# Kernel tuning notes

Hardware: AMD Instinct MI355X
Metric: run time of the kernel (lower is better)

## Reference

```python
import jax, jax.numpy as jnp
import numpy as np

VOCAB = 100000
EMB = 300
B, L = 2048, 256

def setup_inputs() -> dict:
    key = jax.random.key(0)
    k1, k2, k3, k4 = jax.random.split(key, 4)
    tokens = jax.random.randint(k1, (B, L), 0, VOCAB)
    # lengths in [1, L] (original items always have at least one token)
    lengths = jax.random.randint(k2, (B,), 1, L + 1)
    W_emb = jax.random.normal(k3, (VOCAB, EMB), dtype=jnp.float32)
    fc_w = jax.random.normal(k4, (1, EMB), dtype=jnp.float32) / np.sqrt(EMB)
    fc_b = jnp.zeros((1,), dtype=jnp.float32)
    return {"tokens": tokens, "lengths": lengths, "W_emb": W_emb, "fc_w": fc_w, "fc_b": fc_b}

def reference(tokens, lengths, W_emb, fc_w, fc_b):
    # ragged gather + per-item mean pool, fused via padding mask
    emb = W_emb[tokens]                                   # [B, L, D]
    mask = (jnp.arange(L)[None, :] < lengths[:, None])    # [B, L]
    summed = jnp.einsum('bld,bl->bd', emb, mask.astype(emb.dtype))
    avg = summed / lengths[:, None].astype(emb.dtype)     # [B, D]
    z = avg @ fc_w.T + fc_b                               # [B, 1]
    return jax.nn.sigmoid(z)
```

## Files before the change

kernel.cpp:

```cpp
#include <hip/hip_runtime.h>
#include <hip/hip_bf16.h>

#define VOCAB 100000
#define EMB 300
#define BATCH 2048
#define SEQ 256

__global__ void __launch_bounds__(256) vocab_dot_kernel(
    const float* __restrict__ W, const float* __restrict__ fcw,
    float* __restrict__ p, int nrows) {
  const int lane = threadIdx.x & 63;
  const int wave = (blockIdx.x * blockDim.x + threadIdx.x) >> 6;
  const int nwaves = (gridDim.x * blockDim.x) >> 6;

  const float4* fcw4 = (const float4*)fcw;
  float4 wa = fcw4[lane];
  float4 wb = make_float4(0.f, 0.f, 0.f, 0.f);
  if (lane < 11) wb = fcw4[64 + lane];

  for (int v = wave; v < nrows; v += nwaves) {
    const float4* row = (const float4*)(W + (size_t)v * EMB);
    float4 a = row[lane];
    float acc = a.x * wa.x + a.y * wa.y + a.z * wa.z + a.w * wa.w;
    if (lane < 11) {
      float4 b4 = row[64 + lane];
      acc += b4.x * wb.x + b4.y * wb.y + b4.z * wb.z + b4.w * wb.w;
    }
    #pragma unroll
    for (int off = 32; off > 0; off >>= 1)
      acc += __shfl_down(acc, off, 64);
    if (lane == 0) p[v] = acc;
  }
}

__global__ void __launch_bounds__(256) pool_sigmoid_kernel(
    const int* __restrict__ tokens, const int* __restrict__ lengths,
    const float* __restrict__ p, const float* __restrict__ fcb,
    float* __restrict__ out, int B, int L) {
  const int lane = threadIdx.x & 63;
  const int wib = threadIdx.x >> 6;
  const int b = blockIdx.x * (blockDim.x >> 6) + wib;
  if (b >= B) return;

  const int len = lengths[b];
  const int* t = tokens + (size_t)b * L;
  float acc = 0.f;
  for (int l = lane; l < len; l += 64)
    acc += p[t[l]];
  #pragma unroll
  for (int off = 32; off > 0; off >>= 1)
    acc += __shfl_down(acc, off, 64);
  if (lane == 0) {
    float z = acc / (float)len + fcb[0];
    out[b] = 1.0f / (1.0f + expf(-z));
  }
}

extern "C" void kernel_launch(void* const* d_in, const int* in_sizes, int n_in,
                              void* d_out, int out_size, void* d_ws, size_t ws_size,
                              hipStream_t stream) {
  const int*   tokens  = (const int*)d_in[0];
  const int*   lengths = (const int*)d_in[1];
  const float* W_emb   = (const float*)d_in[2];
  const float* fc_w    = (const float*)d_in[3];
  const float* fc_b    = (const float*)d_in[4];
  float* out = (float*)d_out;
  float* p   = (float*)d_ws;

  vocab_dot_kernel<<<2048, 256, 0, stream>>>(W_emb, fc_w, p, VOCAB);

  pool_sigmoid_kernel<<<BATCH / 4, 256, 0, stream>>>(
      tokens, lengths, p, fc_b, out, BATCH, SEQ);
}
```

Baseline: 30.68 us.

## Fuse gather and dot into one per-item pooling kernel, dropping vocab precompute

```diff
diff --git a/kernel.cpp b/kernel.cpp
--- a/kernel.cpp
+++ b/kernel.cpp
@@ -2,56 +2,65 @@
 #include <hip/hip_bf16.h>
 
 #define VOCAB 100000
-#define EMB 300
+#define EMB   300
 #define BATCH 2048
-#define SEQ 256
+#define SEQ   256
 
-__global__ void __launch_bounds__(256) vocab_dot_kernel(
+typedef float f4 __attribute__((ext_vector_type(4)));
+
+__global__ void __launch_bounds__(256) item_pool_kernel(
+    const int* __restrict__ tokens, const int* __restrict__ lengths,
     const float* __restrict__ W, const float* __restrict__ fcw,
-    float* __restrict__ p, int nrows) {
-  const int lane = threadIdx.x & 63;
-  const int wave = (blockIdx.x * blockDim.x + threadIdx.x) >> 6;
-  const int nwaves = (gridDim.x * blockDim.x) >> 6;
+    const float* __restrict__ fcb, float* __restrict__ out) {
+  __shared__ int   stok[SEQ];
+  __shared__ float spart[16];
+  const int b   = blockIdx.x;
+  const int tid = threadIdx.x;
+  const int i   = tid & 15;
+  const int grp = tid >> 4;
+  const int len = lengths[b];
 
-  const float4* fcw4 = (const float4*)fcw;
-  float4 wa = fcw4[lane];
-  float4 wb = make_float4(0.f, 0.f, 0.f, 0.f);
-  if (lane < 11) wb = fcw4[64 + lane];
+  stok[tid] = tokens[(size_t)b * SEQ + tid];
+  __syncthreads();
 
-  for (int v = wave; v < nrows; v += nwaves) {
-    const float4* row = (const float4*)(W + (size_t)v * EMB);
-    float4 a = row[lane];
-    float acc = a.x * wa.x + a.y * wa.y + a.z * wa.z + a.w * wa.w;
-    if (lane < 11) {
-      float4 b4 = row[64 + lane];
-      acc += b4.x * wb.x + b4.y * wb.y + b4.z * wb.z + b4.w * wb.w;
+  const f4* fcw4 = (const f4*)fcw;
+  const f4 zero = {0.f, 0.f, 0.f, 0.f};
+  const f4 w0 = fcw4[i];
+  const f4 w1 = fcw4[i + 16];
+  const f4 w2 = fcw4[i + 32];
+  const f4 w3 = fcw4[i + 48];
+  const f4 w4 = (i < 11) ? fcw4[i + 64] : zero;
+
+  const int nmine = (len > grp) ? ((len - grp + 15) >> 4) : 0;
+
+  f4 acc = zero;
+  if (nmine > 0) {
+    const f4* r = (const f4*)(W + (size_t)stok[grp] * EMB);
+    f4 A0 = r[i], A1 = r[i + 16], A2 = r[i + 32], A3 = r[i + 48];
+    f4 A4 = (i < 11) ? r[i + 64] : zero;
+    #pragma unroll 2
+    for (int j = 1; j < nmine; ++j) {
+      const f4* r2 = (const f4*)(W + (size_t)stok[grp + (j << 4)] * EMB);
+      f4 B0 = r2[i], B1 = r2[i + 16], B2 = r2[i + 32], B3 = r2[i + 48];
+      f4 B4 = (i < 11) ? r2[i + 64] : zero;
+      acc += A0 * w0 + A1 * w1 + A2 * w2 + A3 * w3 + A4 * w4;
+      A0 = B0; A1 = B1; A2 = B2; A3 = B3; A4 = B4;
     }
+    acc += A0 * w0 + A1 * w1 + A2 * w2 + A3 * w3 + A4 * w4;
+  }
+
+  float s = acc.x + acc.y + acc.z + acc.w;
+  s += __shfl_xor(s, 8, 16);
+  s += __shfl_xor(s, 4, 16);
+  s += __shfl_xor(s, 2, 16);
+  s += __shfl_xor(s, 1, 16);
+  if (i == 0) spart[grp] = s;
+  __syncthreads();
+  if (tid == 0) {
+    float t = 0.f;
     #pragma unroll
-    for (int off = 32; off > 0; off >>= 1)
-      acc += __shfl_down(acc, off, 64);
-    if (lane == 0) p[v] = acc;
-  }
-}
-
-__global__ void __launch_bounds__(256) pool_sigmoid_kernel(
-    const int* __restrict__ tokens, const int* __restrict__ lengths,
-    const float* __restrict__ p, const float* __restrict__ fcb,
-    float* __restrict__ out, int B, int L) {
-  const int lane = threadIdx.x & 63;
-  const int wib = threadIdx.x >> 6;
-  const int b = blockIdx.x * (blockDim.x >> 6) + wib;
-  if (b >= B) return;
-
-  const int len = lengths[b];
-  const int* t = tokens + (size_t)b * L;
-  float acc = 0.f;
-  for (int l = lane; l < len; l += 64)
-    acc += p[t[l]];
-  #pragma unroll
-  for (int off = 32; off > 0; off >>= 1)
-    acc += __shfl_down(acc, off, 64);
-  if (lane == 0) {
-    float z = acc / (float)len + fcb[0];
+    for (int k = 0; k < 16; ++k) t += spart[k];
+    const float z = t / (float)len + fcb[0];
     out[b] = 1.0f / (1.0f + expf(-z));
   }
 }
@@ -65,10 +74,7 @@
   const float* fc_w    = (const float*)d_in[3];
   const float* fc_b    = (const float*)d_in[4];
   float* out = (float*)d_out;
-  float* p   = (float*)d_ws;
 
-  vocab_dot_kernel<<<2048, 256, 0, stream>>>(W_emb, fc_w, p, VOCAB);
-
-  pool_sigmoid_kernel<<<BATCH / 4, 256, 0, stream>>>(
-      tokens, lengths, p, fc_b, out, BATCH, SEQ);
+  item_pool_kernel<<<BATCH, 256, 0, stream>>>(
+      tokens, lengths, W_emb, fc_w, fc_b, out);
 }
```

Measured after the change: 54.05 us. 76.1% more time.
